# Kernel tuning notes

Hardware: AMD Instinct MI355X
Metric: run time of the kernel (lower is better)

The kernel has to match this reference:

```python
import jax, jax.numpy as jnp
import numpy as np

NUM_GRAPHS = 64


def setup_inputs() -> dict:
    key = jax.random.key(0)
    ks = jax.random.split(key, 8)
    N, E, H, D_IN, NEXP = 100000, 1600000, 128, 4, 8
    atomic_numbers = jax.random.uniform(ks[0], (N,), dtype=jnp.float32) * 80.0
    pos = jax.random.normal(ks[1], (N, 3), dtype=jnp.float32)
    W0 = jax.random.normal(ks[2], (D_IN, H), dtype=jnp.float32) / np.sqrt(D_IN)
    b0 = jnp.zeros((H,), dtype=jnp.float32)
    W1 = jax.random.normal(ks[3], (H, H), dtype=jnp.float32) / np.sqrt(H)
    b1 = jnp.zeros((H,), dtype=jnp.float32)
    W2 = jax.random.normal(ks[4], (H, H), dtype=jnp.float32) / np.sqrt(H)
    b2 = jnp.zeros((H,), dtype=jnp.float32)
    lin_W = jax.random.normal(ks[5], (H, NEXP), dtype=jnp.float32) / np.sqrt(H)
    lin_b = jnp.zeros((NEXP,), dtype=jnp.float32)
    edge_index = jax.random.randint(ks[6], (2, E), 0, N, dtype=jnp.int64)
    batch = jnp.sort(jax.random.randint(ks[7], (N,), 0, NUM_GRAPHS, dtype=jnp.int64))
    return {
        "atomic_numbers": atomic_numbers, "pos": pos,
        "W0": W0, "b0": b0, "W1": W1, "b1": b1, "W2": W2, "b2": b2,
        "lin_W": lin_W, "lin_b": lin_b,
        "edge_index": edge_index, "batch": batch,
    }


def _gcn_layer(x, W, b, src, dst, norm, num_nodes):
    # GCNConv: transform, then symmetric-normalized scatter-aggregate (self-loops included in src/dst)
    h = x @ W                                   # [N, H]
    msg = h[src] * norm[:, None]                # [E+N, H] edge-gather
    out = jax.ops.segment_sum(msg, dst, num_segments=num_nodes)  # scatter-add at targets
    return out + b


def reference(atomic_numbers, pos, W0, b0, W1, b1, W2, b2, lin_W, lin_b, edge_index, batch):
    N = atomic_numbers.shape[0]
    x = jnp.concatenate([atomic_numbers[:, None], pos], axis=-1)  # [N, 4]

    # add self-loops (PyG GCNConv default)
    loop = jnp.arange(N, dtype=edge_index.dtype)
    src = jnp.concatenate([edge_index[0], loop])
    dst = jnp.concatenate([edge_index[1], loop])
    deg = jax.ops.segment_sum(jnp.ones_like(dst, dtype=jnp.float32), dst, num_segments=N)
    deg_inv_sqrt = jnp.where(deg > 0, deg ** -0.5, 0.0)
    norm = deg_inv_sqrt[src] * deg_inv_sqrt[dst]  # [E+N]

    for (W, b) in ((W0, b0), (W1, b1), (W2, b2)):
        x = _gcn_layer(x, W, b, src, dst, norm, N)
        x = jax.nn.relu(x)
        # dropout is identity at inference

    # global mean pool over graphs
    sums = jax.ops.segment_sum(x, batch, num_segments=NUM_GRAPHS)        # [G, H]
    counts = jax.ops.segment_sum(jnp.ones((N,), jnp.float32), batch, num_segments=NUM_GRAPHS)
    pooled = sums / jnp.maximum(counts, 1.0)[:, None]

    logits = pooled @ lin_W + lin_b             # [G, num_experts]
    return jax.nn.softmax(logits, axis=1)[:, :, None]  # [G, num_experts, 1]
```

## Files before the change

kernel.cpp:

```cpp
#include <hip/hip_runtime.h>
#include <math.h>

#define WG 256
#define NB 256
#define BSHIFT 9
#define NBLK 256

typedef float vf2 __attribute__((ext_vector_type(2)));
typedef short bf16x8 __attribute__((ext_vector_type(8)));
typedef float f32x4 __attribute__((ext_vector_type(4)));

#define XS_STRIDE 136
#define WT_STRIDE 136
#define C_STRIDE 132

__device__ __forceinline__ int lower_bound_i(const int* __restrict__ a, int n, int key) {
    int lo = 0, hi = n;
    while (lo < hi) { int mid = (lo + hi) >> 1; if (a[mid] < key) lo = mid + 1; else hi = mid; }
    return lo;
}

__device__ __forceinline__ void fp8x8_to_f8(uint2 raw, float* f) {
    vf2 a = __builtin_amdgcn_cvt_pk_f32_fp8((int)raw.x, false);
    vf2 b = __builtin_amdgcn_cvt_pk_f32_fp8((int)raw.x, true);
    vf2 c = __builtin_amdgcn_cvt_pk_f32_fp8((int)raw.y, false);
    vf2 d = __builtin_amdgcn_cvt_pk_f32_fp8((int)raw.y, true);
    f[0]=a.x; f[1]=a.y; f[2]=b.x; f[3]=b.y; f[4]=c.x; f[5]=c.y; f[6]=d.x; f[7]=d.y;
}
__device__ __forceinline__ void fp8x16_to_f(uint4 raw, float* f) {
    uint2 lo, hi;
    lo.x = raw.x; lo.y = raw.y; hi.x = raw.z; hi.y = raw.w;
    fp8x8_to_f8(lo, f);
    fp8x8_to_f8(hi, f + 8);
}
__device__ __forceinline__ unsigned int f4_to_fp8x4(float x, float y, float z, float w) {
    int v = __builtin_amdgcn_cvt_pk_fp8_f32(x, y, 0, false);
    v = __builtin_amdgcn_cvt_pk_fp8_f32(z, w, v, true);
    return (unsigned int)v;
}
__device__ __forceinline__ unsigned short f_to_bf_trunc(float f) {
    return (unsigned short)(__float_as_uint(f) >> 16);
}
__device__ __forceinline__ unsigned short f_to_bf_rne(float f) {
    unsigned int u = __float_as_uint(f);
    u += 0x7FFFu + ((u >> 16) & 1u);
    return (unsigned short)(u >> 16);
}


__global__ __launch_bounds__(256) void k_cnt(const int* __restrict__ edst, int E,
                                             int* __restrict__ gcounts) {
    __shared__ int hist[NB];
    int t = threadIdx.x, blk = blockIdx.x;
    if (t < NB) hist[t] = 0;
    __syncthreads();
    int chunk = (E + NBLK - 1) / NBLK;
    int e0 = blk * chunk, e1 = min(E, e0 + chunk);
    for (int e = e0 + t; e < e1; e += 256) atomicAdd(&hist[edst[e] >> BSHIFT], 1);
    __syncthreads();
    if (t < NB) gcounts[t * NBLK + blk] = hist[t];
}

__global__ __launch_bounds__(256) void k_scanA(int* __restrict__ gcounts,
                                               int* __restrict__ bsum) {
    __shared__ int wtot[4];
    int t = threadIdx.x;
    int base = blockIdx.x * 1024 + t * 4;
    int4 v = *(const int4*)&gcounts[base];
    int s = v.x + v.y + v.z + v.w;
    int lane = t & 63, wid = t >> 6;
    int x = s;
#pragma unroll
    for (int d = 1; d < 64; d <<= 1) { int y = __shfl_up(x, d); if (lane >= d) x += y; }
    if (lane == 63) wtot[wid] = x;
    __syncthreads();
    int woff = 0;
    for (int w = 0; w < wid; w++) woff += wtot[w];
    int excl = woff + x - s;
    int4 o;
    o.x = excl; o.y = excl + v.x; o.z = o.y + v.y; o.w = o.z + v.z;
    *(int4*)&gcounts[base] = o;
    if (t == 255) bsum[blockIdx.x] = woff + x;
}

__global__ void k_scanB(int* __restrict__ bsum) {
    int t = threadIdx.x;
    int v = bsum[t];
    int x = v;
#pragma unroll
    for (int d = 1; d < 64; d <<= 1) { int y = __shfl_up(x, d); if (t >= d) x += y; }
    bsum[t] = x - v;
}

__global__ __launch_bounds__(256) void k_scat(const int* __restrict__ esrc,
        const int* __restrict__ edst, int E,
        const int* __restrict__ gcounts, const int* __restrict__ bsum,
        int* __restrict__ pairs) {
    __shared__ int cur[NB];
    int t = threadIdx.x, blk = blockIdx.x;
    if (t < NB) {
        int idx = t * NBLK + blk;
        cur[t] = gcounts[idx] + bsum[idx >> 10];
    }
    __syncthreads();
    int chunk = (E + NBLK - 1) / NBLK;
    int e0 = blk * chunk, e1 = min(E, e0 + chunk);
    for (int e = e0 + t; e < e1; e += 256) {
        int d = edst[e], s = esrc[e];
        int pos = atomicAdd(&cur[d >> BSHIFT], 1);
        pairs[pos] = (s << BSHIFT) | (d & ((1 << BSHIFT) - 1));
    }
}

__global__ __launch_bounds__(256) void k_build(const int* __restrict__ pairs,
        const int* __restrict__ gcounts, const int* __restrict__ bsum, int N, int E,
        int* __restrict__ offs, int* __restrict__ srcs, float* __restrict__ dis) {
    __shared__ int cnt[512];
    __shared__ int wtot[4];
    int b = blockIdx.x, t = threadIdx.x;
    int n0 = b << BSHIFT;
    cnt[2 * t] = 0; cnt[2 * t + 1] = 0;
    __syncthreads();
    int i0 = b * NBLK, i1 = (b + 1) * NBLK;
    int bs = gcounts[i0] + bsum[i0 >> 10];
    int be = gcounts[i1] + bsum[i1 >> 10];
    int m = be - bs;
    const int* pb = &pairs[bs];
    for (int i = t; i < m; i += 256) {
        int p = pb[i];
        atomicAdd(&cnt[p & 511], 1);
    }
    __syncthreads();
    int v0 = cnt[2 * t], v1 = cnt[2 * t + 1];
    int ts = v0 + v1;
    int lane = t & 63, wid = t >> 6;
    int x = ts;
    #pragma unroll
    for (int d = 1; d < 64; d <<= 1) { int y = __shfl_up(x, d); if (lane >= d) x += y; }
    if (lane == 63) wtot[wid] = x;
    __syncthreads();
    int woff = 0;
    for (int w = 0; w < wid; w++) woff += wtot[w];
    int excl = woff + x - ts;
    int o0 = excl, o1 = excl + v0;
    cnt[2 * t] = o0; cnt[2 * t + 1] = o1;
    int n = n0 + 2 * t;
    if (n + 0 < N) { offs[n + 0] = bs + o0; dis[n + 0] = rsqrtf((float)(v0 + 1)); }
    if (n + 1 < N) { offs[n + 1] = bs + o1; dis[n + 1] = rsqrtf((float)(v1 + 1)); }
    if (b == gridDim.x - 1 && t == 255) offs[N] = E;
    __syncthreads();
    for (int i = t; i < m; i += 256) {
        int p = pb[i];
        int pos = atomicAdd(&cnt[p & 511], 1);
        srcs[bs + pos] = p >> BSHIFT;
    }
}

__global__ __launch_bounds__(256) void k_wt(const float* __restrict__ W,
                                            unsigned short* __restrict__ wt) {
    int idx = blockIdx.x * 256 + threadIdx.x;
    int k = idx >> 7, j = idx & 127;
    float v = W[k * 128 + j];
    wt[j * 128 + k] = f_to_bf_rne(v);
}


__global__ void k_l0(const float* __restrict__ an, const float* __restrict__ pos,
                     const float* __restrict__ W0, const float* __restrict__ dis,
                     unsigned int* __restrict__ h, int N) {
    int idx = blockIdx.x * blockDim.x + threadIdx.x;
    int n = idx >> 5, fq = idx & 31;
    if (n >= N) return;
    float a = an[n];
    float px = pos[n * 3 + 0], py = pos[n * 3 + 1], pz = pos[n * 3 + 2];
    float dn = dis[n];
    const float4 w0 = *(const float4*)&W0[0 * 128 + 4 * fq];
    const float4 w1 = *(const float4*)&W0[1 * 128 + 4 * fq];
    const float4 w2 = *(const float4*)&W0[2 * 128 + 4 * fq];
    const float4 w3 = *(const float4*)&W0[3 * 128 + 4 * fq];
    float4 r;
    r.x = (a * w0.x + px * w1.x + py * w2.x + pz * w3.x) * dn;
    r.y = (a * w0.y + px * w1.y + py * w2.y + pz * w3.y) * dn;
    r.z = (a * w0.z + px * w1.z + py * w2.z + pz * w3.z) * dn;
    r.w = (a * w0.w + px * w1.w + py * w2.w + pz * w3.w) * dn;
    h[(size_t)n * 32 + fq] = f4_to_fp8x4(r.x, r.y, r.z, r.w);
}

__global__ __launch_bounds__(256) void k_fused(const unsigned int* __restrict__ x,
        const float* __restrict__ bias, const unsigned short* __restrict__ wt,
        const float* __restrict__ dis, const int* __restrict__ offs,
        const int* __restrict__ srcs, unsigned int* __restrict__ h, int N) {
    __shared__ __align__(16) char ldsb[(64 * XS_STRIDE + 128 * WT_STRIDE) * 2];
    unsigned short* xs  = (unsigned short*)ldsb;
    unsigned short* wtl = xs + 64 * XS_STRIDE;
    float* Cs = (float*)ldsb;

    int t = threadIdx.x;
    int n0 = blockIdx.x * 64;

    {
        const uint4* wg = (const uint4*)wt;
#pragma unroll
        for (int i = 0; i < 8; i++) {
            int idx = t + i * 256;
            int j = idx >> 4, part = idx & 15;
            uint4 v = wg[idx];
            *(uint4*)&wtl[j * WT_STRIDE + part * 8] = v;
        }
    }

    {
        const uint4* hp4 = (const uint4*)x;
        int fq = t & 7, ng = t >> 3;
        float bv[16];
        *(float4*)&bv[0]  = *(const float4*)&bias[fq * 16 + 0];
        *(float4*)&bv[4]  = *(const float4*)&bias[fq * 16 + 4];
        *(float4*)&bv[8]  = *(const float4*)&bias[fq * 16 + 8];
        *(float4*)&bv[12] = *(const float4*)&bias[fq * 16 + 12];
#pragma unroll
        for (int half = 0; half < 2; half++) {
            int lrow = half * 32 + ng;
            int n = n0 + lrow;
            float out[16];
            if (n < N) {
                float acc[16], tmp[16];
                fp8x16_to_f(hp4[(size_t)n * 8 + fq], acc);
                int e0 = offs[n], e1 = offs[n + 1];
                int e = e0;
                for (; e + 4 <= e1; e += 4) {
                    int s0 = srcs[e + 0], s1 = srcs[e + 1];
                    int s2 = srcs[e + 2], s3 = srcs[e + 3];
                    uint4 r0 = hp4[(size_t)s0 * 8 + fq];
                    uint4 r1 = hp4[(size_t)s1 * 8 + fq];
                    uint4 r2 = hp4[(size_t)s2 * 8 + fq];
                    uint4 r3 = hp4[(size_t)s3 * 8 + fq];
                    fp8x16_to_f(r0, tmp);
#pragma unroll
                    for (int k = 0; k < 16; k++) acc[k] += tmp[k];
                    fp8x16_to_f(r1, tmp);
#pragma unroll
                    for (int k = 0; k < 16; k++) acc[k] += tmp[k];
                    fp8x16_to_f(r2, tmp);
#pragma unroll
                    for (int k = 0; k < 16; k++) acc[k] += tmp[k];
                    fp8x16_to_f(r3, tmp);
#pragma unroll
                    for (int k = 0; k < 16; k++) acc[k] += tmp[k];
                }
                for (; e < e1; ++e) {
                    int s = srcs[e];
                    fp8x16_to_f(hp4[(size_t)s * 8 + fq], tmp);
#pragma unroll
                    for (int k = 0; k < 16; k++) acc[k] += tmp[k];
                }
                float dn = dis[n];
#pragma unroll
                for (int k = 0; k < 16; k++) out[k] = fmaxf(bv[k] + dn * acc[k], 0.f);
            } else {
#pragma unroll
                for (int k = 0; k < 16; k++) out[k] = 0.f;
            }
            bf16x8 v0, v1;
#pragma unroll
            for (int k = 0; k < 8; k++) {
                v0[k] = (short)f_to_bf_rne(out[k]);
                v1[k] = (short)f_to_bf_rne(out[k + 8]);
            }
            *(bf16x8*)&xs[lrow * XS_STRIDE + fq * 16] = v0;
            *(bf16x8*)&xs[lrow * XS_STRIDE + fq * 16 + 8] = v1;
        }
    }
    __syncthreads();

    int lane = t & 63, wv = t >> 6;
    int m = lane & 15, quad = lane >> 4;
    int rowbase = wv * 16;

    f32x4 acc[8];
#pragma unroll
    for (int c = 0; c < 8; c++) acc[c] = (f32x4){0.f, 0.f, 0.f, 0.f};

#pragma unroll
    for (int kt = 0; kt < 4; kt++) {
        bf16x8 a = *(bf16x8*)&xs[(rowbase + m) * XS_STRIDE + kt * 32 + quad * 8];
#pragma unroll
        for (int c = 0; c < 8; c++) {
            bf16x8 b = *(bf16x8*)&wtl[(c * 16 + m) * WT_STRIDE + kt * 32 + quad * 8];
            acc[c] = __builtin_amdgcn_mfma_f32_16x16x32_bf16(a, b, acc[c], 0, 0, 0);
        }
    }
    __syncthreads();

#pragma unroll
    for (int c = 0; c < 8; c++) {
#pragma unroll
        for (int r = 0; r < 4; r++) {
            Cs[(rowbase + quad * 4 + r) * C_STRIDE + c * 16 + m] = acc[c][r];
        }
    }
    __syncthreads();

    int fq = t & 31, ng = t >> 5;
#pragma unroll
    for (int i = 0; i < 8; i++) {
        int lrow = ng * 8 + i;
        int n = n0 + lrow;
        if (n < N) {
            float4 v = *(const float4*)&Cs[lrow * C_STRIDE + 4 * fq];
            float dn = dis[n];
            h[(size_t)n * 32 + fq] = f4_to_fp8x4(v.x * dn, v.y * dn, v.z * dn, v.w * dn);
        }
    }
}

__global__ __launch_bounds__(256) void k_agg(const unsigned int* __restrict__ h,
                      const float* __restrict__ bias,
                      const float* __restrict__ dis, const int* __restrict__ offs,
                      const int* __restrict__ srcs, unsigned int* __restrict__ agg, int N) {
    int fq = threadIdx.x & 7, ng = threadIdx.x >> 3;
    int n = blockIdx.x * 32 + ng;
    if (n >= N) return;
    const uint4* hp4 = (const uint4*)h;
    float acc[16], tmp[16];
    fp8x16_to_f(hp4[(size_t)n * 8 + fq], acc);
    int e0 = offs[n], e1 = offs[n + 1];
    int e = e0;
    for (; e + 4 <= e1; e += 4) {
        int s0 = srcs[e + 0], s1 = srcs[e + 1], s2 = srcs[e + 2], s3 = srcs[e + 3];
        uint4 r0 = hp4[(size_t)s0 * 8 + fq];
        uint4 r1 = hp4[(size_t)s1 * 8 + fq];
        uint4 r2 = hp4[(size_t)s2 * 8 + fq];
        uint4 r3 = hp4[(size_t)s3 * 8 + fq];
        fp8x16_to_f(r0, tmp);
#pragma unroll
        for (int k = 0; k < 16; k++) acc[k] += tmp[k];
        fp8x16_to_f(r1, tmp);
#pragma unroll
        for (int k = 0; k < 16; k++) acc[k] += tmp[k];
        fp8x16_to_f(r2, tmp);
#pragma unroll
        for (int k = 0; k < 16; k++) acc[k] += tmp[k];
        fp8x16_to_f(r3, tmp);
#pragma unroll
        for (int k = 0; k < 16; k++) acc[k] += tmp[k];
    }
    for (; e < e1; ++e) {
        int s = srcs[e];
        fp8x16_to_f(hp4[(size_t)s * 8 + fq], tmp);
#pragma unroll
        for (int k = 0; k < 16; k++) acc[k] += tmp[k];
    }
    float dn = dis[n];
    float bv[16];
    *(float4*)&bv[0]  = *(const float4*)&bias[fq * 16 + 0];
    *(float4*)&bv[4]  = *(const float4*)&bias[fq * 16 + 4];
    *(float4*)&bv[8]  = *(const float4*)&bias[fq * 16 + 8];
    *(float4*)&bv[12] = *(const float4*)&bias[fq * 16 + 12];
    float o[16];
#pragma unroll
    for (int k = 0; k < 16; k++) o[k] = bv[k] + dn * acc[k];
    uint4 outv;
    outv.x = f4_to_fp8x4(o[0], o[1], o[2], o[3]);
    outv.y = f4_to_fp8x4(o[4], o[5], o[6], o[7]);
    outv.z = f4_to_fp8x4(o[8], o[9], o[10], o[11]);
    outv.w = f4_to_fp8x4(o[12], o[13], o[14], o[15]);
    *(uint4*)&agg[(size_t)n * 32 + fq * 4] = outv;
}


__global__ void k_pool(const unsigned char* __restrict__ x, const int* __restrict__ batch,
                       float* __restrict__ pooled, int N) {
    int g = blockIdx.x >> 3, c = blockIdx.x & 7;
    int start = lower_bound_i(batch, N, g);
    int end   = lower_bound_i(batch, N, g + 1);
    int len = end - start;
    int cb = start + (int)((long)len * c / 8);
    int ce = start + (int)((long)len * (c + 1) / 8);
    int f = threadIdx.x & 127, half = threadIdx.x >> 7;
    float acc = 0.f;
    for (int n = cb + half; n < ce; n += 2) {
        int b = x[(size_t)n * 128 + f];
        vf2 v = __builtin_amdgcn_cvt_pk_f32_fp8(b, false);
        acc += fmaxf(v.x, 0.f);
    }
    __shared__ float sh[128];
    if (half == 1) sh[f] = acc;
    __syncthreads();
    if (half == 0) atomicAdd(&pooled[g * 128 + f], acc + sh[f]);
}

__global__ void k_head(const float* __restrict__ pooled, const int* __restrict__ batch,
                       const float* __restrict__ linW, const float* __restrict__ linb,
                       float* __restrict__ out, int N) {
    int g = threadIdx.x;
    if (g >= 64) return;
    int start = lower_bound_i(batch, N, g);
    int end   = lower_bound_i(batch, N, g + 1);
    float cnt = fmaxf((float)(end - start), 1.0f);
    float logits[8];
#pragma unroll
    for (int j = 0; j < 8; j++) logits[j] = linb[j];
    for (int f = 0; f < 128; f++) {
        float p = pooled[g * 128 + f] / cnt;
#pragma unroll
        for (int j = 0; j < 8; j++) logits[j] += p * linW[f * 8 + j];
    }
    float m = logits[0];
#pragma unroll
    for (int j = 1; j < 8; j++) m = fmaxf(m, logits[j]);
    float s = 0.f;
    float e[8];
#pragma unroll
    for (int j = 0; j < 8; j++) { e[j] = expf(logits[j] - m); s += e[j]; }
#pragma unroll
    for (int j = 0; j < 8; j++) out[g * 8 + j] = e[j] / s;
}


extern "C" void kernel_launch(void* const* d_in, const int* in_sizes, int n_in,
                              void* d_out, int out_size, void* d_ws, size_t ws_size,
                              hipStream_t stream) {
    const float* an   = (const float*)d_in[0];
    const float* pos  = (const float*)d_in[1];
    const float* W0   = (const float*)d_in[2];
    const float* b0   = (const float*)d_in[3];
    const float* W1   = (const float*)d_in[4];
    const float* b1   = (const float*)d_in[5];
    const float* W2   = (const float*)d_in[6];
    const float* b2   = (const float*)d_in[7];
    const float* linW = (const float*)d_in[8];
    const float* linb = (const float*)d_in[9];
    const int*   ei   = (const int*)d_in[10];
    const int*   batch= (const int*)d_in[11];

    int N = in_sizes[0];
    int E = in_sizes[10] / 2;
    const int* esrc = ei;
    const int* edst = ei + E;
    int nb = (N + (1 << BSHIFT) - 1) >> BSHIFT;

    char* p = (char*)d_ws;
    auto carve = [&](size_t bytes) -> void* {
        void* r = (void*)p;
        p += (bytes + 255) & ~(size_t)255;
        return r;
    };
    unsigned int* bufA = (unsigned int*)carve((size_t)N * 128);
    unsigned int* bufB = (unsigned int*)carve((size_t)N * 128);
    float* dis    = (float*)carve((size_t)N * 4);
    int*   offs   = (int*)  carve((size_t)(N + 1) * 4);
    int*   srcs   = (int*)  carve((size_t)E * 4);
    int*   pairs  = (int*)  carve((size_t)E * 4);
    int*   gcounts= (int*)  carve((size_t)NB * NBLK * 4);
    int*   bsum   = (int*)  carve(64 * 4);
    unsigned short* wt1 = (unsigned short*)carve(128 * 128 * 2);
    unsigned short* wt2 = (unsigned short*)carve(128 * 128 * 2);
    float* pooled = (float*)carve(64 * 128 * 4);

    hipMemsetAsync(pooled, 0, 64 * 128 * 4, stream);

    k_cnt  <<<NBLK, WG, 0, stream>>>(edst, E, gcounts);
    k_scanA<<<(NB * NBLK) / 1024, WG, 0, stream>>>(gcounts, bsum);
    k_scanB<<<1, 64, 0, stream>>>(bsum);
    k_scat <<<NBLK, WG, 0, stream>>>(esrc, edst, E, gcounts, bsum, pairs);
    k_build<<<nb, WG, 0, stream>>>(pairs, gcounts, bsum, N, E, offs, srcs, dis);

    k_wt<<<64, WG, 0, stream>>>(W1, wt1);
    k_wt<<<64, WG, 0, stream>>>(W2, wt2);

    k_l0   <<<((size_t)N * 32 + WG - 1) / WG, WG, 0, stream>>>(an, pos, W0, dis, bufA, N);
    k_fused<<<(N + 63) / 64, WG, 0, stream>>>(bufA, b0, wt1, dis, offs, srcs, bufB, N);
    k_fused<<<(N + 63) / 64, WG, 0, stream>>>(bufB, b1, wt2, dis, offs, srcs, bufA, N);
    k_agg  <<<(N + 31) / 32, WG, 0, stream>>>(bufA, b2, dis, offs, srcs, bufB, N);

    k_pool<<<64 * 8, WG, 0, stream>>>((const unsigned char*)bufB, batch, pooled, N);
    k_head<<<1, 64, 0, stream>>>(pooled, batch, linW, linb, (float*)d_out, N);
}
```

Before: 342.6 us.

## Split fused aggregate+GEMM into separate aggregation and GEMM kernels

Replaces the fused gather-aggregate-then-MFMA kernel with a standalone aggregation kernel (with an 8-wide unrolled gather) followed by a GEMM kernel that reads the fp8 aggregated features, applies ReLU and converts them to bf16 in LDS. The goal is to decouple the latency-bound gather from the LDS-heavy GEMM so each kernel can use its own occupancy and launch shape. The pool kernel now reads four fp8 values per 32-bit load across eight row groups. In exchange there is an extra fp8 round trip through global memory per layer, extra launches, and extra quantization of the aggregated activations to fp8 and then bf16 by truncation.

```diff
diff --git a/kernel.cpp b/kernel.cpp
--- a/kernel.cpp
+++ b/kernel.cpp
@@ -186,10 +186,10 @@
     h[(size_t)n * 32 + fq] = f4_to_fp8x4(r.x, r.y, r.z, r.w);
 }
 
-__global__ __launch_bounds__(256) void k_fused(const unsigned int* __restrict__ x,
-        const float* __restrict__ bias, const unsigned short* __restrict__ wt,
-        const float* __restrict__ dis, const int* __restrict__ offs,
-        const int* __restrict__ srcs, unsigned int* __restrict__ h, int N) {
+__global__ __launch_bounds__(256) void k_gemm(const unsigned int* __restrict__ x,
+                                              const unsigned short* __restrict__ wt,
+                                              const float* __restrict__ dis,
+                                              unsigned int* __restrict__ h, int N) {
     __shared__ __align__(16) char ldsb[(64 * XS_STRIDE + 128 * WT_STRIDE) * 2];
     unsigned short* xs  = (unsigned short*)ldsb;
     unsigned short* wtl = xs + 64 * XS_STRIDE;
@@ -198,6 +198,28 @@
     int t = threadIdx.x;
     int n0 = blockIdx.x * 64;
 
+    {
+        const uint2* xg = (const uint2*)(x + (size_t)n0 * 32);
+        int validq = min(64, N - n0) * 16;
+#pragma unroll
+        for (int i = 0; i < 4; i++) {
+            int idx = t + i * 256;
+            int row = idx >> 4, part = idx & 15;
+            float f[8];
+            if (idx < validq) {
+                fp8x8_to_f8(xg[idx], f);
+#pragma unroll
+                for (int k = 0; k < 8; k++) f[k] = fmaxf(f[k], 0.f);
+            } else {
+#pragma unroll
+                for (int k = 0; k < 8; k++) f[k] = 0.f;
+            }
+            bf16x8 v;
+#pragma unroll
+            for (int k = 0; k < 8; k++) v[k] = (short)f_to_bf_trunc(f[k]);
+            *(bf16x8*)&xs[row * XS_STRIDE + part * 8] = v;
+        }
+    }
     {
         const uint4* wg = (const uint4*)wt;
 #pragma unroll
@@ -206,68 +228,6 @@
             int j = idx >> 4, part = idx & 15;
             uint4 v = wg[idx];
             *(uint4*)&wtl[j * WT_STRIDE + part * 8] = v;
-        }
-    }
-
-    {
-        const uint4* hp4 = (const uint4*)x;
-        int fq = t & 7, ng = t >> 3;
-        float bv[16];
-        *(float4*)&bv[0]  = *(const float4*)&bias[fq * 16 + 0];
-        *(float4*)&bv[4]  = *(const float4*)&bias[fq * 16 + 4];
-        *(float4*)&bv[8]  = *(const float4*)&bias[fq * 16 + 8];
-        *(float4*)&bv[12] = *(const float4*)&bias[fq * 16 + 12];
-#pragma unroll
-        for (int half = 0; half < 2; half++) {
-            int lrow = half * 32 + ng;
-            int n = n0 + lrow;
-            float out[16];
-            if (n < N) {
-                float acc[16], tmp[16];
-                fp8x16_to_f(hp4[(size_t)n * 8 + fq], acc);
-                int e0 = offs[n], e1 = offs[n + 1];
-                int e = e0;
-                for (; e + 4 <= e1; e += 4) {
-                    int s0 = srcs[e + 0], s1 = srcs[e + 1];
-                    int s2 = srcs[e + 2], s3 = srcs[e + 3];
-                    uint4 r0 = hp4[(size_t)s0 * 8 + fq];
-                    uint4 r1 = hp4[(size_t)s1 * 8 + fq];
-                    uint4 r2 = hp4[(size_t)s2 * 8 + fq];
-                    uint4 r3 = hp4[(size_t)s3 * 8 + fq];
-                    fp8x16_to_f(r0, tmp);
-#pragma unroll
-                    for (int k = 0; k < 16; k++) acc[k] += tmp[k];
-                    fp8x16_to_f(r1, tmp);
-#pragma unroll
-                    for (int k = 0; k < 16; k++) acc[k] += tmp[k];
-                    fp8x16_to_f(r2, tmp);
-#pragma unroll
-                    for (int k = 0; k < 16; k++) acc[k] += tmp[k];
-                    fp8x16_to_f(r3, tmp);
-#pragma unroll
-                    for (int k = 0; k < 16; k++) acc[k] += tmp[k];
-                }
-                for (; e < e1; ++e) {
-                    int s = srcs[e];
-                    fp8x16_to_f(hp4[(size_t)s * 8 + fq], tmp);
-#pragma unroll
-                    for (int k = 0; k < 16; k++) acc[k] += tmp[k];
-                }
-                float dn = dis[n];
-#pragma unroll
-                for (int k = 0; k < 16; k++) out[k] = fmaxf(bv[k] + dn * acc[k], 0.f);
-            } else {
-#pragma unroll
-                for (int k = 0; k < 16; k++) out[k] = 0.f;
-            }
-            bf16x8 v0, v1;
-#pragma unroll
-            for (int k = 0; k < 8; k++) {
-                v0[k] = (short)f_to_bf_rne(out[k]);
-                v1[k] = (short)f_to_bf_rne(out[k + 8]);
-            }
-            *(bf16x8*)&xs[lrow * XS_STRIDE + fq * 16] = v0;
-            *(bf16x8*)&xs[lrow * XS_STRIDE + fq * 16 + 8] = v1;
         }
     }
     __syncthreads();
@@ -325,12 +285,45 @@
     fp8x16_to_f(hp4[(size_t)n * 8 + fq], acc);
     int e0 = offs[n], e1 = offs[n + 1];
     int e = e0;
+    for (; e + 8 <= e1; e += 8) {
+        uint4 r0 = hp4[(size_t)srcs[e + 0] * 8 + fq];
+        uint4 r1 = hp4[(size_t)srcs[e + 1] * 8 + fq];
+        uint4 r2 = hp4[(size_t)srcs[e + 2] * 8 + fq];
+        uint4 r3 = hp4[(size_t)srcs[e + 3] * 8 + fq];
+        uint4 r4 = hp4[(size_t)srcs[e + 4] * 8 + fq];
+        uint4 r5 = hp4[(size_t)srcs[e + 5] * 8 + fq];
+        uint4 r6 = hp4[(size_t)srcs[e + 6] * 8 + fq];
+        uint4 r7 = hp4[(size_t)srcs[e + 7] * 8 + fq];
+        fp8x16_to_f(r0, tmp);
+#pragma unroll
+        for (int k = 0; k < 16; k++) acc[k] += tmp[k];
+        fp8x16_to_f(r1, tmp);
+#pragma unroll
+        for (int k = 0; k < 16; k++) acc[k] += tmp[k];
+        fp8x16_to_f(r2, tmp);
+#pragma unroll
+        for (int k = 0; k < 16; k++) acc[k] += tmp[k];
+        fp8x16_to_f(r3, tmp);
+#pragma unroll
+        for (int k = 0; k < 16; k++) acc[k] += tmp[k];
+        fp8x16_to_f(r4, tmp);
+#pragma unroll
+        for (int k = 0; k < 16; k++) acc[k] += tmp[k];
+        fp8x16_to_f(r5, tmp);
+#pragma unroll
+        for (int k = 0; k < 16; k++) acc[k] += tmp[k];
+        fp8x16_to_f(r6, tmp);
+#pragma unroll
+        for (int k = 0; k < 16; k++) acc[k] += tmp[k];
+        fp8x16_to_f(r7, tmp);
+#pragma unroll
+        for (int k = 0; k < 16; k++) acc[k] += tmp[k];
+    }
     for (; e + 4 <= e1; e += 4) {
-        int s0 = srcs[e + 0], s1 = srcs[e + 1], s2 = srcs[e + 2], s3 = srcs[e + 3];
-        uint4 r0 = hp4[(size_t)s0 * 8 + fq];
-        uint4 r1 = hp4[(size_t)s1 * 8 + fq];
-        uint4 r2 = hp4[(size_t)s2 * 8 + fq];
-        uint4 r3 = hp4[(size_t)s3 * 8 + fq];
+        uint4 r0 = hp4[(size_t)srcs[e + 0] * 8 + fq];
+        uint4 r1 = hp4[(size_t)srcs[e + 1] * 8 + fq];
+        uint4 r2 = hp4[(size_t)srcs[e + 2] * 8 + fq];
+        uint4 r3 = hp4[(size_t)srcs[e + 3] * 8 + fq];
         fp8x16_to_f(r0, tmp);
 #pragma unroll
         for (int k = 0; k < 16; k++) acc[k] += tmp[k];
@@ -345,8 +338,7 @@
         for (int k = 0; k < 16; k++) acc[k] += tmp[k];
     }
     for (; e < e1; ++e) {
-        int s = srcs[e];
-        fp8x16_to_f(hp4[(size_t)s * 8 + fq], tmp);
+        fp8x16_to_f(hp4[(size_t)srcs[e] * 8 + fq], tmp);
 #pragma unroll
         for (int k = 0; k < 16; k++) acc[k] += tmp[k];
     }
@@ -368,7 +360,7 @@
 }
 
 
-__global__ void k_pool(const unsigned char* __restrict__ x, const int* __restrict__ batch,
+__global__ void k_pool(const unsigned int* __restrict__ x, const int* __restrict__ batch,
                        float* __restrict__ pooled, int N) {
     int g = blockIdx.x >> 3, c = blockIdx.x & 7;
     int start = lower_bound_i(batch, N, g);
@@ -376,17 +368,26 @@
     int len = end - start;
     int cb = start + (int)((long)len * c / 8);
     int ce = start + (int)((long)len * (c + 1) / 8);
-    int f = threadIdx.x & 127, half = threadIdx.x >> 7;
-    float acc = 0.f;
-    for (int n = cb + half; n < ce; n += 2) {
-        int b = x[(size_t)n * 128 + f];
-        vf2 v = __builtin_amdgcn_cvt_pk_f32_fp8(b, false);
-        acc += fmaxf(v.x, 0.f);
-    }
-    __shared__ float sh[128];
-    if (half == 1) sh[f] = acc;
-    __syncthreads();
-    if (half == 0) atomicAdd(&pooled[g * 128 + f], acc + sh[f]);
+    int fq = threadIdx.x & 31, rg = threadIdx.x >> 5;
+    float acc[4] = {0.f, 0.f, 0.f, 0.f};
+    for (int n = cb + rg; n < ce; n += 8) {
+        unsigned int u = x[(size_t)n * 32 + fq];
+        vf2 lo = __builtin_amdgcn_cvt_pk_f32_fp8((int)u, false);
+        vf2 hi = __builtin_amdgcn_cvt_pk_f32_fp8((int)u, true);
+        acc[0] += fmaxf(lo.x, 0.f); acc[1] += fmaxf(lo.y, 0.f);
+        acc[2] += fmaxf(hi.x, 0.f); acc[3] += fmaxf(hi.y, 0.f);
+    }
+    __shared__ float sh[8 * 128];
+#pragma unroll
+    for (int k = 0; k < 4; k++) sh[rg * 128 + fq * 4 + k] = acc[k];
+    __syncthreads();
+    int t = threadIdx.x;
+    if (t < 128) {
+        float s = 0.f;
+#pragma unroll
+        for (int r = 0; r < 8; r++) s += sh[r * 128 + t];
+        atomicAdd(&pooled[g * 128 + t], s);
+    }
 }
 
 __global__ void k_head(const float* __restrict__ pooled, const int* __restrict__ batch,
@@ -468,11 +469,13 @@
     k_wt<<<64, WG, 0, stream>>>(W1, wt1);
     k_wt<<<64, WG, 0, stream>>>(W2, wt2);
 
-    k_l0   <<<((size_t)N * 32 + WG - 1) / WG, WG, 0, stream>>>(an, pos, W0, dis, bufA, N);
-    k_fused<<<(N + 63) / 64, WG, 0, stream>>>(bufA, b0, wt1, dis, offs, srcs, bufB, N);
-    k_fused<<<(N + 63) / 64, WG, 0, stream>>>(bufB, b1, wt2, dis, offs, srcs, bufA, N);
-    k_agg  <<<(N + 31) / 32, WG, 0, stream>>>(bufA, b2, dis, offs, srcs, bufB, N);
-
-    k_pool<<<64 * 8, WG, 0, stream>>>((const unsigned char*)bufB, batch, pooled, N);
+    k_l0  <<<((size_t)N * 32 + WG - 1) / WG, WG, 0, stream>>>(an, pos, W0, dis, bufA, N);
+    k_agg <<<(N + 31) / 32, WG, 0, stream>>>(bufA, b0, dis, offs, srcs, bufB, N);
+    k_gemm<<<(N + 63) / 64, WG, 0, stream>>>(bufB, wt1, dis, bufA, N);
+    k_agg <<<(N + 31) / 32, WG, 0, stream>>>(bufA, b1, dis, offs, srcs, bufB, N);
+    k_gemm<<<(N + 63) / 64, WG, 0, stream>>>(bufB, wt2, dis, bufA, N);
+    k_agg <<<(N + 31) / 32, WG, 0, stream>>>(bufA, b2, dis, offs, srcs, bufB, N);
+
+    k_pool<<<64 * 8, WG, 0, stream>>>(bufB, batch, pooled, N);
     k_head<<<1, 64, 0, stream>>>(pooled, batch, linW, linb, (float*)d_out, N);
 }
```

New measurement: 330.2 us. -3.6%, faster.
